# Kernel tuning notes

Hardware: AMD Instinct MI355X
Metric: run time of the kernel (lower is better)

The kernel has to match this reference:

```python
import jax, jax.numpy as jnp
import numpy as np

B, S, D = 2, 2048, 1024
H = 16
DH = D // H


def setup_inputs() -> dict:
    key = jax.random.key(0)
    ks = jax.random.split(key, 6)
    scale = 1.0 / np.sqrt(D)
    x = jax.random.normal(ks[0], (B, S, D), dtype=jnp.float32)
    Wq = jax.random.normal(ks[1], (D, D), dtype=jnp.float32) * scale
    Wk = jax.random.normal(ks[2], (D, D), dtype=jnp.float32) * scale
    Wv = jax.random.normal(ks[3], (D, D), dtype=jnp.float32) * scale
    Wo = jax.random.normal(ks[4], (D, D), dtype=jnp.float32) * scale
    bo = jax.random.normal(ks[5], (D,), dtype=jnp.float32) * 0.01
    return {"x": x, "Wq": Wq, "Wk": Wk, "Wv": Wv, "Wo": Wo, "bo": bo}


def reference(x, Wq, Wk, Wv, Wo, bo):
    b, t, _ = x.shape
    # project and split heads: [b, h, t, dh]
    q = (x @ Wq).reshape(b, t, H, DH).transpose(0, 2, 1, 3)
    k = (x @ Wk).reshape(b, t, H, DH).transpose(0, 2, 1, 3)
    v = (x @ Wv).reshape(b, t, H, DH).transpose(0, 2, 1, 3)
    scores = jnp.einsum('bhqd,bhkd->bhqk', q, k)
    causal = jnp.triu(jnp.ones((t, t), dtype=bool), k=1)
    scores = jnp.where(causal, -jnp.inf, scores)
    attn = jax.nn.softmax(scores / np.sqrt(DH), axis=-1)
    ctx = jnp.einsum('bhqk,bhkd->bhqd', attn, v)
    ctx = ctx.transpose(0, 2, 1, 3).reshape(b, t, D)
    return ctx @ Wo + bo
```

## Files before the change

kernel.cpp:

```cpp
#include <hip/hip_runtime.h>
#include <hip/hip_bf16.h>

#define B 2
#define S 2048
#define D 1024
#define NH 16
#define DH 64
#define M (B*S)
#define BQ 64
#define BK 64
#define KSCALE 0.18033688011112042f

typedef __hip_bfloat16 bf16;
typedef __attribute__((ext_vector_type(8))) short frag_ab;
typedef __attribute__((ext_vector_type(4))) float frag_cd;
typedef unsigned long long ull;

__device__ __forceinline__ void gload_lds16(const bf16* g, bf16* l) {
    __builtin_amdgcn_global_load_lds((const __attribute__((address_space(1))) unsigned int*)g,
                                     (__attribute__((address_space(3))) unsigned int*)l,
                                     16, 0, 0);
}

__global__ __launch_bounds__(256) void prep(const float* __restrict__ x,  bf16* __restrict__ xb,
                                            const float* __restrict__ W0, const float* __restrict__ W1,
                                            const float* __restrict__ W2, const float* __restrict__ W3,
                                            bf16* __restrict__ T0, bf16* __restrict__ T1,
                                            bf16* __restrict__ T2, bf16* __restrict__ T3) {
    if (blockIdx.z == 4) {
        const int l = blockIdx.y * 32 + blockIdx.x;
        int i = (l * 256 + threadIdx.x) * 4;
#pragma unroll
        for (int rep = 0; rep < 4; rep++, i += 1024 * 256 * 4) {
            const float4 v = *(const float4*)(x + i);
            __align__(8) bf16 t4[4] = {__float2bfloat16(v.x), __float2bfloat16(v.y),
                                       __float2bfloat16(v.z), __float2bfloat16(v.w)};
            *(ull*)(xb + i) = *(const ull*)t4;
        }
        return;
    }
    const float* src; bf16* dst;
    switch (blockIdx.z) {
        case 0: src = W0; dst = T0; break;
        case 1: src = W1; dst = T1; break;
        case 2: src = W2; dst = T2; break;
        default: src = W3; dst = T3; break;
    }
    __shared__ float t[32][33];
    const int tx = threadIdx.x & 31, ty = threadIdx.x >> 5;
    const int c0 = blockIdx.x * 32, r0 = blockIdx.y * 32;
#pragma unroll
    for (int i = 0; i < 4; i++)
        t[ty + 8 * i][tx] = src[(size_t)(r0 + ty + 8 * i) * D + c0 + tx];
    __syncthreads();
#pragma unroll
    for (int i = 0; i < 4; i++)
        dst[(size_t)(c0 + ty + 8 * i) * D + r0 + tx] = __float2bfloat16(t[tx][ty + 8 * i]);
}

__global__ __launch_bounds__(256) void gemm_qkv_all(const bf16* __restrict__ A, const bf16* __restrict__ Bt,
                                                    bf16* __restrict__ Qb, bf16* __restrict__ Kb,
                                                    bf16* __restrict__ Vt_g) {
    __shared__ __align__(16) bf16 As[128 * BK];
    __shared__ __align__(16) bf16 Bs[128 * BK];
    const int tid = threadIdx.x, wave = tid >> 6, lane = tid & 63;
    const int r16 = lane & 15, quad = lane >> 4;
    const int row0 = blockIdx.y * 128;
    const int col0 = blockIdx.x * 128;
    const int wm = (wave & 1) * 64, wn = (wave >> 1) * 64;

    frag_cd acc[4][4];
#pragma unroll
    for (int mt = 0; mt < 4; mt++)
#pragma unroll
        for (int nt = 0; nt < 4; nt++) acc[mt][nt] = frag_cd{0.f, 0.f, 0.f, 0.f};

    for (int k0 = 0; k0 < D; k0 += BK) {
        __syncthreads();
#pragma unroll
        for (int j = 0; j < 4; j++) {
            const int s = wave * 256 + j * 64 + lane;
            const int r = s >> 3;
            const int c = (s ^ r) & 7;
            gload_lds16(A  + (size_t)(row0 + r) * D + k0 + c * 8, &As[(wave * 256 + j * 64) * 8]);
            gload_lds16(Bt + (size_t)(col0 + r) * D + k0 + c * 8, &Bs[(wave * 256 + j * 64) * 8]);
        }
        __syncthreads();

        frag_ab af[4][2], bf[4][2];
#pragma unroll
        for (int mt = 0; mt < 4; mt++) {
            const int row = wm + mt * 16 + r16;
#pragma unroll
            for (int ks = 0; ks < 2; ks++)
                af[mt][ks] = *(const frag_ab*)&As[row * 64 + (((ks * 4 + quad) ^ (row & 7)) * 8)];
        }
#pragma unroll
        for (int nt = 0; nt < 4; nt++) {
            const int row = wn + nt * 16 + r16;
#pragma unroll
            for (int ks = 0; ks < 2; ks++)
                bf[nt][ks] = *(const frag_ab*)&Bs[row * 64 + (((ks * 4 + quad) ^ (row & 7)) * 8)];
        }
#pragma unroll
        for (int mt = 0; mt < 4; mt++)
#pragma unroll
            for (int nt = 0; nt < 4; nt++)
#pragma unroll
                for (int ks = 0; ks < 2; ks++)
                    acc[mt][nt] = __builtin_amdgcn_mfma_f32_16x16x32_bf16(
                        af[mt][ks], bf[nt][ks], acc[mt][nt], 0, 0, 0);
    }

    const int third = col0 >> 10;
    if (third < 2) {
        bf16* Out = (third == 0) ? Qb : Kb;
        const float sc = (third == 0) ? KSCALE : 1.f;
#pragma unroll
        for (int mt = 0; mt < 4; mt++)
#pragma unroll
            for (int nt = 0; nt < 4; nt++) {
                const int cl = (col0 + wn + nt * 16 + r16) & 1023;
#pragma unroll
                for (int rg = 0; rg < 4; rg++) {
                    const int row = row0 + wm + mt * 16 + quad * 4 + rg;
                    Out[(size_t)row * D + cl] = __float2bfloat16(acc[mt][nt][rg] * sc);
                }
            }
    } else {
        const int bb = row0 >> 11;
        const int sb0 = (row0 & 2047) + wm;
#pragma unroll
        for (int mt = 0; mt < 4; mt++)
#pragma unroll
            for (int nt = 0; nt < 4; nt++) {
                const int c  = (col0 + wn + nt * 16 + r16) - 2048;
                const int hh = c >> 6, dl = c & 63;
                const int sb = sb0 + mt * 16 + quad * 4;
                __align__(8) bf16 t4[4];
#pragma unroll
                for (int rg = 0; rg < 4; rg++) t4[rg] = __float2bfloat16(acc[mt][nt][rg]);
                *(ull*)(Vt_g + (((size_t)bb * 16 + hh) * 64 + dl) * S + sb) = *(const ull*)t4;
            }
    }
}

__global__ __launch_bounds__(256, 3) void attn_mfma(const bf16* __restrict__ Q,
                                                    const bf16* __restrict__ K,
                                                    const bf16* __restrict__ Vg,
                                                    bf16* __restrict__ Ctx) {
    __shared__ __align__(16) bf16 Ks[2][BK * DH];
    __shared__ __align__(16) bf16 Vt[2][BK * DH];
    __shared__ float lred[4 * BQ];

    const int tid = threadIdx.x, wave = tid >> 6, lane = tid & 63;
    const int r16 = lane & 15, quad = lane >> 4;
    const int bh = blockIdx.x, jy = blockIdx.y;
    const int qt = (jy < 16) ? jy : 47 - jy;
    const int b = bh >> 4, h = bh & 15;
    const size_t base  = (size_t)b * S * D + (size_t)h * DH;
    const size_t vbase = (size_t)bh * DH * S;
    const int q0 = qt * BQ;
    const int nkt = qt + 1;
    const int wkey = wave * 16;

#pragma unroll
    for (int j = 0; j < 2; j++) {
        const int s = wave * 128 + j * 64 + lane;
        const int r = s >> 3, c = (s ^ r) & 7;
        gload_lds16(K  + base  + (size_t)r * D + c * 8, &Ks[0][(wave * 128 + j * 64) * 8]);
        gload_lds16(Vg + vbase + (size_t)r * S + c * 8, &Vt[0][(wave * 128 + j * 64) * 8]);
    }

    frag_ab qf[4][2];
#pragma unroll
    for (int qb = 0; qb < 4; qb++) {
        const bf16* qp = Q + base + (size_t)(q0 + qb * 16 + r16) * D + quad * 8;
#pragma unroll
        for (int ks = 0; ks < 2; ks++)
            qf[qb][ks] = *(const frag_ab*)(qp + ks * 32);
    }
    __syncthreads();

    frag_cd Oacc[4][4];
#pragma unroll
    for (int nd = 0; nd < 4; nd++)
#pragma unroll
        for (int qb = 0; qb < 4; qb++) Oacc[nd][qb] = frag_cd{0.f, 0.f, 0.f, 0.f};
    float lsum[4] = {0.f, 0.f, 0.f, 0.f};

    for (int kt = 0; kt < nkt; kt++) {
        const int k0  = kt * BK;
        const int cur = kt & 1;

        if (kt + 1 < nkt) {
            const int kn = k0 + BK;
#pragma unroll
            for (int j = 0; j < 2; j++) {
                const int s = wave * 128 + j * 64 + lane;
                const int r = s >> 3, c = (s ^ r) & 7;
                gload_lds16(K  + base  + (size_t)(kn + r) * D + c * 8,
                            &Ks[cur ^ 1][(wave * 128 + j * 64) * 8]);
                gload_lds16(Vg + vbase + (size_t)r * S + kn + c * 8,
                            &Vt[cur ^ 1][(wave * 128 + j * 64) * 8]);
            }
        }

        const int krow = wkey + r16;
        frag_ab ka[2];
#pragma unroll
        for (int ks = 0; ks < 2; ks++)
            ka[ks] = *(const frag_ab*)&Ks[cur][krow * 64 + (((ks * 4 + quad) ^ (krow & 7)) * 8)];

        frag_ab pbf[4];
        const int keyg = k0 + wkey + quad * 4;
#pragma unroll
        for (int qb = 0; qb < 4; qb++) {
            frag_cd Sc = frag_cd{0.f, 0.f, 0.f, 0.f};
#pragma unroll
            for (int ks = 0; ks < 2; ks++)
                Sc = __builtin_amdgcn_mfma_f32_16x16x32_bf16(ka[ks], qf[qb][ks], Sc, 0, 0, 0);
            const bool msk = (k0 + wkey + 15) > (q0 + qb * 16);
            const int qg = q0 + qb * 16 + r16;
            float p[4];
#pragma unroll
            for (int rg = 0; rg < 4; rg++) {
                float sv = Sc[rg];
                if (msk) sv = (keyg + rg <= qg) ? sv : -1e30f;
                p[rg] = __builtin_amdgcn_exp2f(sv);
            }
            lsum[qb] += (p[0] + p[1]) + (p[2] + p[3]);
            __align__(8) bf16 t4[4] = {__float2bfloat16(p[0]), __float2bfloat16(p[1]),
                                       __float2bfloat16(p[2]), __float2bfloat16(p[3])};
            union { ull u[2]; frag_ab f; } tp;
            tp.u[0] = *(const ull*)t4;
            tp.u[1] = 0ull;
            pbf[qb] = tp.f;
        }

#pragma unroll
        for (int nd = 0; nd < 4; nd++) {
            const int vrow = nd * 16 + r16;
            const int slot = ((wkey + quad * 4) >> 3) ^ (vrow & 7);
            union { ull u[2]; frag_ab f; } tv;
            tv.u[0] = *(const ull*)&Vt[cur][vrow * 64 + slot * 8 + (quad & 1) * 4];
            tv.u[1] = tv.u[0];
#pragma unroll
            for (int qb = 0; qb < 4; qb++)
                Oacc[nd][qb] = __builtin_amdgcn_mfma_f32_16x16x32_bf16(
                    tv.f, pbf[qb], Oacc[nd][qb], 0, 0, 0);
        }

        __syncthreads();
    }

#pragma unroll
    for (int qb = 0; qb < 4; qb++) {
        lsum[qb] += __shfl_xor(lsum[qb], 16, 64);
        lsum[qb] += __shfl_xor(lsum[qb], 32, 64);
    }
    if (quad == 0) {
#pragma unroll
        for (int qb = 0; qb < 4; qb++)
            lred[wave * 64 + qb * 16 + r16] = lsum[qb];
    }

    float* red0 = (float*)&Ks[0][0];
    float* red1 = (float*)&Vt[0][0];
    if (wave >= 2) {
        float* red = (wave == 2) ? red0 : red1;
#pragma unroll
        for (int nd = 0; nd < 4; nd++)
#pragma unroll
            for (int qb = 0; qb < 4; qb++) {
                const int idx = (qb * 16 + r16) * 64 + (((nd * 4 + quad) ^ (r16 & 7)) * 4);
                *(float4*)&red[idx] = float4{Oacc[nd][qb][0], Oacc[nd][qb][1],
                                             Oacc[nd][qb][2], Oacc[nd][qb][3]};
            }
    }
    __syncthreads();
    if (wave < 2) {
        float* red = (wave == 0) ? red0 : red1;
#pragma unroll
        for (int nd = 0; nd < 4; nd++)
#pragma unroll
            for (int qb = 0; qb < 4; qb++) {
                const int idx = (qb * 16 + r16) * 64 + (((nd * 4 + quad) ^ (r16 & 7)) * 4);
                const float4 v = *(const float4*)&red[idx];
#pragma unroll
                for (int rg = 0; rg < 4; rg++) Oacc[nd][qb][rg] += ((const float*)&v)[rg];
            }
    }
    __syncthreads();
    if (wave == 1) {
#pragma unroll
        for (int nd = 0; nd < 4; nd++)
#pragma unroll
            for (int qb = 0; qb < 4; qb++) {
                const int idx = (qb * 16 + r16) * 64 + (((nd * 4 + quad) ^ (r16 & 7)) * 4);
                *(float4*)&red0[idx] = float4{Oacc[nd][qb][0], Oacc[nd][qb][1],
                                              Oacc[nd][qb][2], Oacc[nd][qb][3]};
            }
    }
    __syncthreads();
    if (wave == 0) {
        float lt[4];
#pragma unroll
        for (int qb = 0; qb < 4; qb++) {
            const int qi = qb * 16 + r16;
            lt[qb] = 1.f / (lred[qi] + lred[64 + qi] + lred[128 + qi] + lred[192 + qi]);
        }
#pragma unroll
        for (int nd = 0; nd < 4; nd++)
#pragma unroll
            for (int qb = 0; qb < 4; qb++) {
                const int idx = (qb * 16 + r16) * 64 + (((nd * 4 + quad) ^ (r16 & 7)) * 4);
                const float4 v = *(const float4*)&red0[idx];
                __align__(8) bf16 t4[4];
#pragma unroll
                for (int rg = 0; rg < 4; rg++)
                    t4[rg] = __float2bfloat16((Oacc[nd][qb][rg] + ((const float*)&v)[rg]) * lt[qb]);
                *(ull*)(Ctx + base + (size_t)(q0 + qb * 16 + r16) * D + nd * 16 + quad * 4) =
                    *(const ull*)t4;
            }
    }
}

__global__ __launch_bounds__(256) void gemm_out64(const bf16* __restrict__ A, const bf16* __restrict__ Bt,
                                                  const float* __restrict__ bias, float* __restrict__ Out) {
    __shared__ __align__(16) bf16 As[2][64 * BK];
    __shared__ __align__(16) bf16 Bs[2][128 * BK];
    const int tid = threadIdx.x, wave = tid >> 6, lane = tid & 63;
    const int r16 = lane & 15, quad = lane >> 4;
    const int row0 = blockIdx.y * 64;
    const int col0 = blockIdx.x * 128;
    const int wm = (wave & 1) * 32, wn = (wave >> 1) * 64;

    frag_cd acc[2][4];
#pragma unroll
    for (int mt = 0; mt < 2; mt++)
#pragma unroll
        for (int nt = 0; nt < 4; nt++) acc[mt][nt] = frag_cd{0.f, 0.f, 0.f, 0.f};

#pragma unroll
    for (int j = 0; j < 2; j++) {
        const int s = wave * 128 + j * 64 + lane;
        const int r = s >> 3, c = (s ^ r) & 7;
        gload_lds16(A + (size_t)(row0 + r) * D + c * 8, &As[0][(wave * 128 + j * 64) * 8]);
    }
#pragma unroll
    for (int j = 0; j < 4; j++) {
        const int s = wave * 256 + j * 64 + lane;
        const int r = s >> 3, c = (s ^ r) & 7;
        gload_lds16(Bt + (size_t)(col0 + r) * D + c * 8, &Bs[0][(wave * 256 + j * 64) * 8]);
    }
    __syncthreads();

    for (int kt = 0; kt < D / BK; kt++) {
        const int cur = kt & 1;
        if (kt + 1 < D / BK) {
            const int kn = (kt + 1) * BK;
#pragma unroll
            for (int j = 0; j < 2; j++) {
                const int s = wave * 128 + j * 64 + lane;
                const int r = s >> 3, c = (s ^ r) & 7;
                gload_lds16(A + (size_t)(row0 + r) * D + kn + c * 8,
                            &As[cur ^ 1][(wave * 128 + j * 64) * 8]);
            }
#pragma unroll
            for (int j = 0; j < 4; j++) {
                const int s = wave * 256 + j * 64 + lane;
                const int r = s >> 3, c = (s ^ r) & 7;
                gload_lds16(Bt + (size_t)(col0 + r) * D + kn + c * 8,
                            &Bs[cur ^ 1][(wave * 256 + j * 64) * 8]);
            }
        }

        frag_ab af[2][2], bf[4][2];
#pragma unroll
        for (int mt = 0; mt < 2; mt++) {
            const int row = wm + mt * 16 + r16;
#pragma unroll
            for (int ks = 0; ks < 2; ks++)
                af[mt][ks] = *(const frag_ab*)&As[cur][row * 64 + (((ks * 4 + quad) ^ (row & 7)) * 8)];
        }
#pragma unroll
        for (int nt = 0; nt < 4; nt++) {
            const int row = wn + nt * 16 + r16;
#pragma unroll
            for (int ks = 0; ks < 2; ks++)
                bf[nt][ks] = *(const frag_ab*)&Bs[cur][row * 64 + (((ks * 4 + quad) ^ (row & 7)) * 8)];
        }
#pragma unroll
        for (int mt = 0; mt < 2; mt++)
#pragma unroll
            for (int nt = 0; nt < 4; nt++)
#pragma unroll
                for (int ks = 0; ks < 2; ks++)
                    acc[mt][nt] = __builtin_amdgcn_mfma_f32_16x16x32_bf16(
                        af[mt][ks], bf[nt][ks], acc[mt][nt], 0, 0, 0);

        __syncthreads();
    }

#pragma unroll
    for (int mt = 0; mt < 2; mt++)
#pragma unroll
        for (int nt = 0; nt < 4; nt++) {
            const int col = col0 + wn + nt * 16 + r16;
            const float bv = bias[col];
#pragma unroll
            for (int rg = 0; rg < 4; rg++) {
                const int row = row0 + wm + mt * 16 + quad * 4 + rg;
                Out[(size_t)row * D + col] = acc[mt][nt][rg] + bv;
            }
        }
}

extern "C" void kernel_launch(void* const* d_in, const int* in_sizes, int n_in,
                              void* d_out, int out_size, void* d_ws, size_t ws_size,
                              hipStream_t stream) {
    const float* x  = (const float*)d_in[0];
    const float* Wq = (const float*)d_in[1];
    const float* Wk = (const float*)d_in[2];
    const float* Wv = (const float*)d_in[3];
    const float* Wo = (const float*)d_in[4];
    const float* bo = (const float*)d_in[5];
    float* out = (float*)d_out;

    bf16* xb    = (bf16*)d_ws;
    bf16* WqkvT = xb    + (size_t)M * D;
    bf16* WoT   = WqkvT + (size_t)3 * D * D;
    bf16* Qb    = WoT   + (size_t)D * D;
    bf16* Kb    = Qb    + (size_t)M * D;
    bf16* Vt_g  = Kb    + (size_t)M * D;
    bf16* Ctxb  = Vt_g  + (size_t)M * D;

    prep<<<dim3(32, 32, 5), 256, 0, stream>>>(x, xb, Wq, Wk, Wv, Wo,
                                              WqkvT, WqkvT + (size_t)D * D,
                                              WqkvT + (size_t)2 * D * D, WoT);
    gemm_qkv_all<<<dim3(24, 32), 256, 0, stream>>>(xb, WqkvT, Qb, Kb, Vt_g);
    attn_mfma<<<dim3(B * NH, S / BQ), 256, 0, stream>>>(Qb, Kb, Vt_g, Ctxb);
    gemm_out64<<<dim3(8, 64), 256, 0, stream>>>(Ctxb, WoT, bo, out);
}
```

Baseline: 179.3 us.

## Process two key tiles per iteration with full-K MFMA and MFMA row sums

Restructures the attention loop so each iteration stages two 64-key tiles, with wave pairs splitting them by tile and key half. Each wave now feeds full 32-key MFMA operands instead of zero-padded halves, and V is staged in an MFMA-friendly layout. Row sums of P are computed with an MFMA against a ones vector instead of VALU adds and shuffles. The query-tile schedule is reversed so heavy tiles launch first. Occupancy drops to 2 blocks per CU because LDS doubles.

```diff
diff --git a/kernel.cpp b/kernel.cpp
--- a/kernel.cpp
+++ b/kernel.cpp
@@ -145,33 +145,48 @@
     }
 }
 
-__global__ __launch_bounds__(256, 3) void attn_mfma(const bf16* __restrict__ Q,
+__global__ __launch_bounds__(256, 2) void attn_mfma(const bf16* __restrict__ Q,
                                                     const bf16* __restrict__ K,
                                                     const bf16* __restrict__ Vg,
                                                     bf16* __restrict__ Ctx) {
-    __shared__ __align__(16) bf16 Ks[2][BK * DH];
-    __shared__ __align__(16) bf16 Vt[2][BK * DH];
+    __shared__ __align__(16) bf16 Ks[2][2][BK * DH];
+    __shared__ __align__(16) bf16 Vt[2][2][BK * DH];
     __shared__ float lred[4 * BQ];
 
     const int tid = threadIdx.x, wave = tid >> 6, lane = tid & 63;
     const int r16 = lane & 15, quad = lane >> 4;
     const int bh = blockIdx.x, jy = blockIdx.y;
-    const int qt = (jy < 16) ? jy : 47 - jy;
+    const int qt = (jy < 16) ? 31 - jy : jy - 16;
     const int b = bh >> 4, h = bh & 15;
     const size_t base  = (size_t)b * S * D + (size_t)h * DH;
     const size_t vbase = (size_t)bh * DH * S;
     const int q0 = qt * BQ;
     const int nkt = qt + 1;
-    const int wkey = wave * 16;
-
-#pragma unroll
-    for (int j = 0; j < 2; j++) {
-        const int s = wave * 128 + j * 64 + lane;
-        const int r = s >> 3, c = (s ^ r) & 7;
-        gload_lds16(K  + base  + (size_t)r * D + c * 8, &Ks[0][(wave * 128 + j * 64) * 8]);
-        gload_lds16(Vg + vbase + (size_t)r * S + c * 8, &Vt[0][(wave * 128 + j * 64) * 8]);
-    }
-
+    const int nchunk = (nkt + 1) >> 1;
+    const int hv = wave & 1;
+    const int tsel = wave >> 1;
+
+    auto STAGE_TILE = [&](int buf, int ti, int t64) {
+#pragma unroll
+        for (int j = 0; j < 2; j++) {
+            const int s = wave * 128 + j * 64 + lane;
+            const int r = s >> 3, c = (s ^ r) & 7;
+            gload_lds16(K + base + (size_t)(t64 * 64 + r) * D + c * 8,
+                        &Ks[buf][ti][(wave * 128 + j * 64) * 8]);
+        }
+#pragma unroll
+        for (int j = 0; j < 2; j++) {
+            const int s = wave * 128 + j * 64 + lane;
+            const int a = s & 1, dloc = (s >> 1) & 15, rk = (s >> 5) & 7, hvs = s >> 8;
+            const int nd = rk >> 1, kb = rk & 1;
+            gload_lds16(Vg + vbase + (size_t)(nd * 16 + dloc) * S
+                           + t64 * 64 + hvs * 32 + kb * 16 + a * 8,
+                        &Vt[buf][ti][(wave * 128 + j * 64) * 8]);
+        }
+    };
+
+    STAGE_TILE(0, 0, 0);
+    if (1 < nkt) STAGE_TILE(0, 1, 1);
     frag_ab qf[4][2];
 #pragma unroll
     for (int qb = 0; qb < 4; qb++) {
@@ -182,91 +197,97 @@
     }
     __syncthreads();
 
+    const frag_ab onesf = {(short)0x3F80, (short)0x3F80, (short)0x3F80, (short)0x3F80,
+                           (short)0x3F80, (short)0x3F80, (short)0x3F80, (short)0x3F80};
+
     frag_cd Oacc[4][4];
+    frag_cd Lacc[4];
 #pragma unroll
     for (int nd = 0; nd < 4; nd++)
 #pragma unroll
         for (int qb = 0; qb < 4; qb++) Oacc[nd][qb] = frag_cd{0.f, 0.f, 0.f, 0.f};
-    float lsum[4] = {0.f, 0.f, 0.f, 0.f};
-
-    for (int kt = 0; kt < nkt; kt++) {
-        const int k0  = kt * BK;
-        const int cur = kt & 1;
-
-        if (kt + 1 < nkt) {
-            const int kn = k0 + BK;
-#pragma unroll
-            for (int j = 0; j < 2; j++) {
-                const int s = wave * 128 + j * 64 + lane;
-                const int r = s >> 3, c = (s ^ r) & 7;
-                gload_lds16(K  + base  + (size_t)(kn + r) * D + c * 8,
-                            &Ks[cur ^ 1][(wave * 128 + j * 64) * 8]);
-                gload_lds16(Vg + vbase + (size_t)r * S + kn + c * 8,
-                            &Vt[cur ^ 1][(wave * 128 + j * 64) * 8]);
-            }
-        }
-
-        const int krow = wkey + r16;
-        frag_ab ka[2];
-#pragma unroll
-        for (int ks = 0; ks < 2; ks++)
-            ka[ks] = *(const frag_ab*)&Ks[cur][krow * 64 + (((ks * 4 + quad) ^ (krow & 7)) * 8)];
-
-        frag_ab pbf[4];
-        const int keyg = k0 + wkey + quad * 4;
-#pragma unroll
-        for (int qb = 0; qb < 4; qb++) {
-            frag_cd Sc = frag_cd{0.f, 0.f, 0.f, 0.f};
-#pragma unroll
-            for (int ks = 0; ks < 2; ks++)
-                Sc = __builtin_amdgcn_mfma_f32_16x16x32_bf16(ka[ks], qf[qb][ks], Sc, 0, 0, 0);
-            const bool msk = (k0 + wkey + 15) > (q0 + qb * 16);
-            const int qg = q0 + qb * 16 + r16;
-            float p[4];
-#pragma unroll
-            for (int rg = 0; rg < 4; rg++) {
-                float sv = Sc[rg];
-                if (msk) sv = (keyg + rg <= qg) ? sv : -1e30f;
-                p[rg] = __builtin_amdgcn_exp2f(sv);
-            }
-            lsum[qb] += (p[0] + p[1]) + (p[2] + p[3]);
-            __align__(8) bf16 t4[4] = {__float2bfloat16(p[0]), __float2bfloat16(p[1]),
-                                       __float2bfloat16(p[2]), __float2bfloat16(p[3])};
-            union { ull u[2]; frag_ab f; } tp;
-            tp.u[0] = *(const ull*)t4;
-            tp.u[1] = 0ull;
-            pbf[qb] = tp.f;
-        }
-
-#pragma unroll
-        for (int nd = 0; nd < 4; nd++) {
-            const int vrow = nd * 16 + r16;
-            const int slot = ((wkey + quad * 4) >> 3) ^ (vrow & 7);
-            union { ull u[2]; frag_ab f; } tv;
-            tv.u[0] = *(const ull*)&Vt[cur][vrow * 64 + slot * 8 + (quad & 1) * 4];
-            tv.u[1] = tv.u[0];
-#pragma unroll
-            for (int qb = 0; qb < 4; qb++)
-                Oacc[nd][qb] = __builtin_amdgcn_mfma_f32_16x16x32_bf16(
-                    tv.f, pbf[qb], Oacc[nd][qb], 0, 0, 0);
+#pragma unroll
+    for (int qb = 0; qb < 4; qb++) Lacc[qb] = frag_cd{0.f, 0.f, 0.f, 0.f};
+
+    for (int c = 0; c < nchunk; c++) {
+        const int cur = c & 1;
+        if (c + 1 < nchunk) {
+            const int t64a = (c + 1) * 2;
+            STAGE_TILE(cur ^ 1, 0, t64a);
+            if (t64a + 1 < nkt) STAGE_TILE(cur ^ 1, 1, t64a + 1);
+        }
+
+        const int k64 = c * 2 + tsel;
+        if (k64 < nkt) {
+            frag_ab ka[2][2];
+#pragma unroll
+            for (int mk = 0; mk < 2; mk++) {
+                const int row = hv * 32 + mk * 16 + r16;
+#pragma unroll
+                for (int ks = 0; ks < 2; ks++)
+                    ka[mk][ks] = *(const frag_ab*)
+                        &Ks[cur][tsel][row * 64 + (((ks * 4 + quad) ^ (row & 7)) * 8)];
+            }
+            ull vb[4][2];
+#pragma unroll
+            for (int nd = 0; nd < 4; nd++)
+#pragma unroll
+                for (int kb = 0; kb < 2; kb++)
+                    vb[nd][kb] = *(const ull*)
+                        &Vt[cur][tsel][hv * 2048 + ((nd * 2 + kb) * 16 + r16) * 16 + quad * 4];
+
+            const bool dm = (k64 == qt);
+            frag_ab pbf[4];
+#pragma unroll
+            for (int qb = 0; qb < 4; qb++) {
+                frag_cd Sc[2];
+                Sc[0] = frag_cd{0.f, 0.f, 0.f, 0.f};
+                Sc[1] = frag_cd{0.f, 0.f, 0.f, 0.f};
+#pragma unroll
+                for (int ks = 0; ks < 2; ks++) {
+                    Sc[0] = __builtin_amdgcn_mfma_f32_16x16x32_bf16(ka[0][ks], qf[qb][ks], Sc[0], 0, 0, 0);
+                    Sc[1] = __builtin_amdgcn_mfma_f32_16x16x32_bf16(ka[1][ks], qf[qb][ks], Sc[1], 0, 0, 0);
+                }
+                __align__(16) bf16 t8[8];
+#pragma unroll
+                for (int mk = 0; mk < 2; mk++)
+#pragma unroll
+                    for (int rg = 0; rg < 4; rg++) {
+                        float sv = Sc[mk][rg];
+                        if (dm) {
+                            const int keyl = hv * 32 + mk * 16 + quad * 4 + rg;
+                            const int ql   = qb * 16 + r16;
+                            sv = (keyl <= ql) ? sv : -1e30f;
+                        }
+                        t8[mk * 4 + rg] = __float2bfloat16(__builtin_amdgcn_exp2f(sv));
+                    }
+                pbf[qb] = *(const frag_ab*)t8;
+                Lacc[qb] = __builtin_amdgcn_mfma_f32_16x16x32_bf16(onesf, pbf[qb], Lacc[qb], 0, 0, 0);
+            }
+
+#pragma unroll
+            for (int nd = 0; nd < 4; nd++) {
+                union { ull u[2]; frag_ab f; } tv;
+                tv.u[0] = vb[nd][0];
+                tv.u[1] = vb[nd][1];
+#pragma unroll
+                for (int qb = 0; qb < 4; qb++)
+                    Oacc[nd][qb] = __builtin_amdgcn_mfma_f32_16x16x32_bf16(
+                        tv.f, pbf[qb], Oacc[nd][qb], 0, 0, 0);
+            }
         }
 
         __syncthreads();
     }
 
-#pragma unroll
-    for (int qb = 0; qb < 4; qb++) {
-        lsum[qb] += __shfl_xor(lsum[qb], 16, 64);
-        lsum[qb] += __shfl_xor(lsum[qb], 32, 64);
-    }
     if (quad == 0) {
 #pragma unroll
         for (int qb = 0; qb < 4; qb++)
-            lred[wave * 64 + qb * 16 + r16] = lsum[qb];
-    }
-
-    float* red0 = (float*)&Ks[0][0];
-    float* red1 = (float*)&Vt[0][0];
+            lred[wave * 64 + qb * 16 + r16] = Lacc[qb][0];
+    }
+
+    float* red0 = (float*)&Ks[0][0][0];
+    float* red1 = (float*)&Vt[0][0][0];
     if (wave >= 2) {
         float* red = (wave == 2) ? red0 : red1;
 #pragma unroll
```

Result: no change. 179.4 us (+0.1%).
